# Performance work log

Hardware: AMD Instinct MI355X
Metric: run time of the kernel (lower is better)

## Reference

```python
import jax, jax.numpy as jnp
import numpy as np
from jax import lax

B, L = 4, 1024
D_MODEL = 512
D_INNER = 2 * D_MODEL            # expand=2 -> 1024
HEADDIM = 64
NHEADS = D_INNER // HEADDIM      # 16
D_STATE = 64
D_CONV = 4
NLAYERS = 2
NTOKEN = 60695
PAD_IDX = 60694
NCLS = 164
CONV_DIM = D_INNER + 2 * D_STATE            # 1152 (ngroups=1)
D_IN_PROJ = 2 * D_INNER + 2 * D_STATE + NHEADS  # 2192
MAX_VALUE = 512.0
EPS = 1e-5


def _ln(x, g=None, b=None):
    m = jnp.mean(x, -1, keepdims=True)
    v = jnp.mean((x - m) ** 2, -1, keepdims=True)
    y = (x - m) * lax.rsqrt(v + EPS)
    return y if g is None else y * g + b


def _smart_flip(X, pad_mask):
    # reverse only the valid (non-pad) prefix of each sequence
    lengths = (~pad_mask).sum(1)
    rng = jnp.arange(X.shape[1])[None, :]
    flip = rng < lengths[:, None]
    pos = jnp.where(flip, lengths[:, None] - 1 - rng, rng)
    return jnp.take_along_axis(X, pos[:, :, None], axis=1)


def _mamba2(u, in_w, conv_w, conv_b, A_log, dt_bias, Dskip, norm_w, out_w):
    # Mamba2 block (mamba_ssm defaults: ngroups=1, silu conv act, gated RMSNorm)
    Bb, Ll, _ = u.shape
    zxbcdt = u @ in_w.T                                      # (B,L,D_IN_PROJ)
    z = zxbcdt[..., :D_INNER]
    xBC = zxbcdt[..., D_INNER:D_INNER + CONV_DIM]
    dt = jax.nn.softplus(zxbcdt[..., -NHEADS:] + dt_bias)    # (B,L,H)
    # causal depthwise conv1d + silu
    xBC = jnp.pad(xBC, ((0, 0), (D_CONV - 1, 0), (0, 0))).transpose(0, 2, 1)
    xBC = lax.conv_general_dilated(xBC, conv_w[:, None, :], (1,), 'VALID',
                                   feature_group_count=CONV_DIM)
    xBC = jax.nn.silu(xBC.transpose(0, 2, 1) + conv_b)       # (B,L,CONV_DIM)
    x = xBC[..., :D_INNER].reshape(Bb, Ll, NHEADS, HEADDIM)
    Bm = xBC[..., D_INNER:D_INNER + D_STATE]                 # (B,L,N)
    Cm = xBC[..., D_INNER + D_STATE:]                        # (B,L,N)
    dA = jnp.exp(dt * (-jnp.exp(A_log)))                     # (B,L,H)

    def step(h, t):
        dA_t, dt_t, x_t, B_t, C_t = t
        # h: (B,H,P,N)
        h = h * dA_t[:, :, None, None] \
            + (dt_t[:, :, None] * x_t)[..., None] * B_t[:, None, None, :]
        y = jnp.einsum('bhpn,bn->bhp', h, C_t)
        return h, y

    h0 = jnp.zeros((Bb, NHEADS, HEADDIM, D_STATE), u.dtype)
    xs = (dA.transpose(1, 0, 2), dt.transpose(1, 0, 2),
          x.transpose(1, 0, 2, 3), Bm.transpose(1, 0, 2), Cm.transpose(1, 0, 2))
    _, ys = lax.scan(step, h0, xs)                            # (L,B,H,P)
    y = ys.transpose(1, 0, 2, 3) + Dskip[None, None, :, None] * x
    y = y.reshape(Bb, Ll, D_INNER)
    y = y * jax.nn.silu(z)                                    # gated RMSNorm
    y = y * lax.rsqrt(jnp.mean(y * y, -1, keepdims=True) + EPS) * norm_w
    return y @ out_w.T


def _forward(src, values, pad_mask, embed, ge_ln_g, ge_ln_b,
             ve_w1, ve_b1, ve_w2, ve_b2, ve_ln_g, ve_ln_b,
             in_proj_w, conv_w_f, conv_b_f, A_log_f, dt_bias_f, D_f, norm_w_f,
             conv_w_r, conv_b_r, A_log_r, dt_bias_r, D_r, norm_w_r, out_proj_w,
             expr_w1, expr_b1, expr_w2, expr_b2, expr_w3, expr_b3,
             cls_w1, cls_b1, cls_ln1_g, cls_ln1_b, cls_w2, cls_b2,
             cls_ln2_g, cls_ln2_b, cls_wo, cls_bo):
    src_emb = _ln(embed[src], ge_ln_g, ge_ln_b)
    v = jnp.minimum(values, MAX_VALUE)[..., None]
    v = jax.nn.relu(v @ ve_w1.T + ve_b1)
    v = _ln(v @ ve_w2.T + ve_b2, ve_ln_g, ve_ln_b)
    h = (src_emb + v) * (~pad_mask)[..., None]
    for i in range(NLAYERS):
        hn = _ln(h)  # F.layer_norm without affine
        out = _mamba2(hn, in_proj_w[i], conv_w_f[i], conv_b_f[i], A_log_f[i],
                      dt_bias_f[i], D_f[i], norm_w_f[i], out_proj_w[i])
        rev = _smart_flip(hn, pad_mask)
        out_r = _mamba2(rev, in_proj_w[i], conv_w_r[i], conv_b_r[i], A_log_r[i],
                        dt_bias_r[i], D_r[i], norm_w_r[i], out_proj_w[i])
        out_r = _smart_flip(out_r, pad_mask)
        h = _ln((out + out_r) / 2)
    # ExprDecoder (MLM head)
    e = jax.nn.leaky_relu(h @ expr_w1.T + expr_b1)
    e = jax.nn.leaky_relu(e @ expr_w2.T + expr_b2)
    mlm = (e @ expr_w3.T + expr_b3)[..., 0]
    # cell embedding: cls token
    cell = h[:, 0, :]
    # ClsDecoder
    c = _ln(jax.nn.relu(cell @ cls_w1.T + cls_b1), cls_ln1_g, cls_ln1_b)
    c = _ln(jax.nn.relu(c @ cls_w2.T + cls_b2), cls_ln2_g, cls_ln2_b)
    cls = c @ cls_wo.T + cls_bo
    return mlm, cell, cls


def setup_inputs() -> dict:
    key = jax.random.key(0)
    ks = iter(jax.random.split(key, 64))
    w = lambda *s: jax.random.normal(next(ks), s, jnp.float32) * 0.02
    embed = w(NTOKEN, D_MODEL).at[PAD_IDX].set(0.0)
    dt_u = jax.random.uniform(next(ks), (NLAYERS, NHEADS), minval=1e-3, maxval=0.1)
    dt_u2 = jax.random.uniform(next(ks), (NLAYERS, NHEADS), minval=1e-3, maxval=0.1)
    return dict(
        src=jax.random.randint(next(ks), (B, L), 0, PAD_IDX),
        values=jax.random.uniform(next(ks), (B, L), jnp.float32),
        src_key_padding_mask=jnp.zeros((B, L), bool),
        embed=embed,
        ge_ln_g=jnp.ones((D_MODEL,)), ge_ln_b=jnp.zeros((D_MODEL,)),
        ve_w1=w(D_MODEL, 1), ve_b1=jnp.zeros((D_MODEL,)),
        ve_w2=w(D_MODEL, D_MODEL), ve_b2=jnp.zeros((D_MODEL,)),
        ve_ln_g=jnp.ones((D_MODEL,)), ve_ln_b=jnp.zeros((D_MODEL,)),
        in_proj_w=w(NLAYERS, D_IN_PROJ, D_MODEL),
        conv_w_f=w(NLAYERS, CONV_DIM, D_CONV), conv_b_f=jnp.zeros((NLAYERS, CONV_DIM)),
        A_log_f=jnp.log(jax.random.uniform(next(ks), (NLAYERS, NHEADS), minval=1.0, maxval=16.0)),
        dt_bias_f=dt_u + jnp.log(-jnp.expm1(-dt_u)),
        D_f=jnp.ones((NLAYERS, NHEADS)), norm_w_f=jnp.ones((NLAYERS, D_INNER)),
        conv_w_r=w(NLAYERS, CONV_DIM, D_CONV), conv_b_r=jnp.zeros((NLAYERS, CONV_DIM)),
        A_log_r=jnp.log(jax.random.uniform(next(ks), (NLAYERS, NHEADS), minval=1.0, maxval=16.0)),
        dt_bias_r=dt_u2 + jnp.log(-jnp.expm1(-dt_u2)),
        D_r=jnp.ones((NLAYERS, NHEADS)), norm_w_r=jnp.ones((NLAYERS, D_INNER)),
        out_proj_w=w(NLAYERS, D_MODEL, D_INNER),
        expr_w1=w(D_MODEL, D_MODEL), expr_b1=jnp.zeros((D_MODEL,)),
        expr_w2=w(D_MODEL, D_MODEL), expr_b2=jnp.zeros((D_MODEL,)),
        expr_w3=w(1, D_MODEL), expr_b3=jnp.zeros((1,)),
        cls_w1=w(D_MODEL, D_MODEL), cls_b1=jnp.zeros((D_MODEL,)),
        cls_ln1_g=jnp.ones((D_MODEL,)), cls_ln1_b=jnp.zeros((D_MODEL,)),
        cls_w2=w(D_MODEL, D_MODEL), cls_b2=jnp.zeros((D_MODEL,)),
        cls_ln2_g=jnp.ones((D_MODEL,)), cls_ln2_b=jnp.zeros((D_MODEL,)),
        cls_wo=w(NCLS, D_MODEL), cls_bo=jnp.zeros((NCLS,)),
    )


def reference(src, values, src_key_padding_mask, embed, ge_ln_g, ge_ln_b,
              ve_w1, ve_b1, ve_w2, ve_b2, ve_ln_g, ve_ln_b,
              in_proj_w, conv_w_f, conv_b_f, A_log_f, dt_bias_f, D_f, norm_w_f,
              conv_w_r, conv_b_r, A_log_r, dt_bias_r, D_r, norm_w_r, out_proj_w,
              expr_w1, expr_b1, expr_w2, expr_b2, expr_w3, expr_b3,
              cls_w1, cls_b1, cls_ln1_g, cls_ln1_b, cls_w2, cls_b2,
              cls_ln2_g, cls_ln2_b, cls_wo, cls_bo):
    return _forward(src, values, src_key_padding_mask, embed, ge_ln_g, ge_ln_b,
                    ve_w1, ve_b1, ve_w2, ve_b2, ve_ln_g, ve_ln_b,
                    in_proj_w, conv_w_f, conv_b_f, A_log_f, dt_bias_f, D_f, norm_w_f,
                    conv_w_r, conv_b_r, A_log_r, dt_bias_r, D_r, norm_w_r, out_proj_w,
                    expr_w1, expr_b1, expr_w2, expr_b2, expr_w3, expr_b3,
                    cls_w1, cls_b1, cls_ln1_g, cls_ln1_b, cls_w2, cls_b2,
                    cls_ln2_g, cls_ln2_b, cls_wo, cls_bo)
```

## Files before the change

kernel.cpp:

```cpp
#include <hip/hip_runtime.h>
#include <hip/hip_bf16.h>
#include <math.h>

constexpr int Bb = 4, Ls = 1024, DM = 512, DI = 1024, NH = 16, HD = 64, DS = 64;
constexpr int CDIM = DI + 2 * DS;
constexpr int DIP  = 2 * DI + 2 * DS + NH;
constexpr int NPJ  = 2 * DI + 2 * DS;
constexpr float EPSf = 1e-5f;
constexpr int TOK = Bb * Ls;
constexpr int CH = 64, NCH = Ls / CH;

#define DEVI __device__ __forceinline__

using bfrag = __attribute__((ext_vector_type(8))) short;
using f4v   = __attribute__((ext_vector_type(4))) float;
using u16x8 = __attribute__((ext_vector_type(8))) unsigned short;

#define GLOAD16(gp, lp)                                                              \
  __builtin_amdgcn_global_load_lds((__attribute__((address_space(1))) void*)(gp),   \
                                   (__attribute__((address_space(3))) void*)(lp),   \
                                   16, 0, 0)

DEVI float wsum(float v) {
#pragma unroll
  for (int o = 32; o > 0; o >>= 1) v += __shfl_xor(v, o);
  return v;
}
DEVI float sigmoidf_(float x) { return 1.f / (1.f + __expf(-x)); }
DEVI unsigned short f2bf(float x) {
  union { float f; unsigned u; } c{x};
  unsigned u = c.u;
  u += 0x7fffu + ((u >> 16) & 1u);
  return (unsigned short)(u >> 16);
}
DEVI float bf2f(unsigned short u) {
  union { unsigned u; float f; } c{(unsigned)u << 16};
  return c.f;
}

DEVI void ld8(const float* __restrict__ p, int lane, float (&x)[8]) {
  float4 a = *(const float4*)(p + lane * 4);
  float4 b = *(const float4*)(p + 256 + lane * 4);
  x[0] = a.x; x[1] = a.y; x[2] = a.z; x[3] = a.w;
  x[4] = b.x; x[5] = b.y; x[6] = b.z; x[7] = b.w;
}
DEVI void ld8bf(const unsigned short* __restrict__ p, int lane, float (&x)[8]) {
  ushort4 a = *(const ushort4*)(p + lane * 4);
  ushort4 b = *(const ushort4*)(p + 256 + lane * 4);
  x[0] = bf2f(a.x); x[1] = bf2f(a.y); x[2] = bf2f(a.z); x[3] = bf2f(a.w);
  x[4] = bf2f(b.x); x[5] = bf2f(b.y); x[6] = bf2f(b.z); x[7] = bf2f(b.w);
}
DEVI void st8(float* __restrict__ p, int lane, const float (&x)[8]) {
  *(float4*)(p + lane * 4) = make_float4(x[0], x[1], x[2], x[3]);
  *(float4*)(p + 256 + lane * 4) = make_float4(x[4], x[5], x[6], x[7]);
}
DEVI void st8bf(unsigned short* __restrict__ p, int lane, const float (&x)[8]) {
  *(ushort4*)(p + lane * 4) = make_ushort4(f2bf(x[0]), f2bf(x[1]), f2bf(x[2]), f2bf(x[3]));
  *(ushort4*)(p + 256 + lane * 4) = make_ushort4(f2bf(x[4]), f2bf(x[5]), f2bf(x[6]), f2bf(x[7]));
}
DEVI void norm8(float (&x)[8]) {
  float s = 0;
#pragma unroll
  for (int j = 0; j < 8; ++j) s += x[j];
  float mean = wsum(s) * (1.f / 512.f);
#pragma unroll
  for (int j = 0; j < 8; ++j) x[j] -= mean;
  float q = 0;
#pragma unroll
  for (int j = 0; j < 8; ++j) q += x[j] * x[j];
  float var = wsum(q) * (1.f / 512.f);
  float inv = rsqrtf(var + EPSf);
#pragma unroll
  for (int j = 0; j < 8; ++j) x[j] *= inv;
}

__global__ __launch_bounds__(256) void k_w2bf(const float* __restrict__ in,
                                              unsigned short* __restrict__ out, int n8) {
  int i = blockIdx.x * 256 + threadIdx.x;
  if (i >= n8) return;
  const float4* p = (const float4*)in + (size_t)i * 2;
  float4 a = p[0], b = p[1];
  *((ushort4*)out + (size_t)i * 2) = make_ushort4(f2bf(a.x), f2bf(a.y), f2bf(a.z), f2bf(a.w));
  *((ushort4*)out + (size_t)i * 2 + 1) = make_ushort4(f2bf(b.x), f2bf(b.y), f2bf(b.z), f2bf(b.w));
}

__global__ __launch_bounds__(256) void k_embed(const int* __restrict__ src, const float* __restrict__ values,
    const float* __restrict__ embed, const float* __restrict__ gg, const float* __restrict__ gb,
    const float* __restrict__ vw1, const float* __restrict__ vb1,
    float* __restrict__ hbuf, unsigned short* __restrict__ v1bf) {
  int gw = (blockIdx.x * 256 + threadIdx.x) >> 6;
  int lane = threadIdx.x & 63;
  if (gw >= TOK) return;
  const float* er = embed + (size_t)src[gw] * DM;
  float x[8];
  ld8(er, lane, x);
  norm8(x);
  float g[8], bv[8];
  ld8(gg, lane, g); ld8(gb, lane, bv);
#pragma unroll
  for (int j = 0; j < 8; ++j) x[j] = x[j] * g[j] + bv[j];
  st8(hbuf + (size_t)gw * DM, lane, x);
  float val = fminf(values[gw], 512.f);
  float w1[8], b1[8];
  ld8(vw1, lane, w1); ld8(vb1, lane, b1);
  float v[8];
#pragma unroll
  for (int j = 0; j < 8; ++j) v[j] = fmaxf(val * w1[j] + b1[j], 0.f);
  st8bf(v1bf + (size_t)gw * DM, lane, v);
}

__global__ __launch_bounds__(256) void k_haddv(const float* __restrict__ t2, const float* __restrict__ g,
    const float* __restrict__ bb, const unsigned char* __restrict__ mask, float* __restrict__ hbuf) {
  int gw = (blockIdx.x * 256 + threadIdx.x) >> 6;
  int lane = threadIdx.x & 63;
  if (gw >= TOK) return;
  float x[8];
  ld8(t2 + (size_t)gw * DM, lane, x);
  norm8(x);
  float gv[8], bv[8], h[8];
  ld8(g, lane, gv); ld8(bb, lane, bv);
  ld8(hbuf + (size_t)gw * DM, lane, h);
  float mf = mask[gw] ? 0.f : 1.f;
#pragma unroll
  for (int j = 0; j < 8; ++j) h[j] = (h[j] + x[j] * gv[j] + bv[j]) * mf;
  st8(hbuf + (size_t)gw * DM, lane, h);
}

__global__ __launch_bounds__(256) void k_lndt(const float* __restrict__ h, const float* __restrict__ inw,
    const float* __restrict__ dtbF, const float* __restrict__ AlogF,
    const float* __restrict__ dtbR, const float* __restrict__ AlogR,
    const int* __restrict__ len, unsigned short* __restrict__ hnbf,
    float* __restrict__ dtf, float* __restrict__ laf,
    float* __restrict__ dtr, float* __restrict__ lar) {
  int gw = (blockIdx.x * 256 + threadIdx.x) >> 6;
  int lane = threadIdx.x & 63;
  if (gw >= TOK) return;
  float x[8];
  ld8(h + (size_t)gw * DM, lane, x);
  norm8(x);
  st8bf(hnbf + (size_t)gw * DM, lane, x);
  const float* wdt = inw + (size_t)NPJ * DM;
  float myraw = 0.f;
#pragma unroll
  for (int hh = 0; hh < NH; ++hh) {
    float w[8];
    ld8(wdt + (size_t)hh * DM, lane, w);
    float s = 0;
#pragma unroll
    for (int j = 0; j < 8; ++j) s += x[j] * w[j];
    s = wsum(s);
    if (lane == hh) myraw = s;
  }
  if (lane < NH) {
    int t = gw & (Ls - 1), b = gw >> 10;
    int ln = len[b];
    int pos = (t < ln) ? (ln - 1 - t) : t;
    size_t grev = (size_t)(b * Ls + pos);
    float rf = myraw + dtbF[lane];
    float df = rf > 20.f ? rf : log1pf(__expf(rf));
    dtf[(size_t)gw * NH + lane] = df;
    laf[(size_t)gw * NH + lane] = -__expf(AlogF[lane]) * df;
    float rr = myraw + dtbR[lane];
    float dr = rr > 20.f ? rr : log1pf(__expf(rr));
    dtr[grev * NH + lane] = dr;
    lar[grev * NH + lane] = -__expf(AlogR[lane]) * dr;
  }
}

template <int ACT, int OMODE>
__global__ __launch_bounds__(256) void gemm_bf(const unsigned short* __restrict__ A,
    const unsigned short* __restrict__ W, const float* __restrict__ bias,
    void* __restrict__ Cout, int M, int N, int K) {
  constexpr int BK = 64;
  __shared__ unsigned short As[128 * BK];
  __shared__ unsigned short Bs[128 * BK];
  int tid = threadIdx.x;
  int bm = blockIdx.y * 128, bn = blockIdx.x * 128;
  int wv = tid >> 6, lane = tid & 63;
  int mb = (wv >> 1) * 64, nb = (wv & 1) * 64;
  int rA = lane >> 3;
  int cswz = (lane & 7) ^ rA;
  f4v acc[4][4] = {};

  for (int k0 = 0; k0 < K; k0 += BK) {
#pragma unroll
    for (int q = 0; q < 4; ++q) {
      int ch = wv * 4 + q;
      const unsigned short* ga = A + (size_t)(bm + ch * 8 + rA) * K + k0 + cswz * 8;
      GLOAD16(ga, &As[ch * 512]);
      const unsigned short* gb = W + (size_t)(bn + ch * 8 + rA) * K + k0 + cswz * 8;
      GLOAD16(gb, &Bs[ch * 512]);
    }
    __syncthreads();
#pragma unroll
    for (int ks = 0; ks < BK; ks += 32) {
      int kb = (ks >> 3) + (lane >> 4);
      bfrag af[4], bg[4];
#pragma unroll
      for (int i = 0; i < 4; ++i) {
        int ra_ = mb + i * 16 + (lane & 15);
        af[i] = *(const bfrag*)((const char*)As + ((ra_ * 128 + kb * 16) ^ ((ra_ & 7) << 4)));
        int rb_ = nb + i * 16 + (lane & 15);
        bg[i] = *(const bfrag*)((const char*)Bs + ((rb_ * 128 + kb * 16) ^ ((rb_ & 7) << 4)));
      }
#pragma unroll
      for (int i = 0; i < 4; ++i)
#pragma unroll
        for (int j = 0; j < 4; ++j)
          acc[i][j] = __builtin_amdgcn_mfma_f32_16x16x32_bf16(af[i], bg[j], acc[i][j], 0, 0, 0);
    }
    __syncthreads();
  }

  int cb = bn + nb + (lane & 15);
  int rb = bm + mb + ((lane >> 4) << 2);
#pragma unroll
  for (int j = 0; j < 4; ++j) {
    float bv = bias ? bias[cb + j * 16] : 0.f;
#pragma unroll
    for (int i = 0; i < 4; ++i) {
#pragma unroll
      for (int r = 0; r < 4; ++r) {
        float v = acc[i][j][r] + bv;
        if (ACT == 1) v = fmaxf(v, 0.f);
        if (ACT == 2) v = v > 0.f ? v : 0.01f * v;
        size_t idx = (size_t)(rb + i * 16 + r) * N + cb + j * 16;
        if (OMODE == 0) ((float*)Cout)[idx] = v;
        else ((unsigned short*)Cout)[idx] = f2bf(v);
      }
    }
  }
}

__global__ __launch_bounds__(256) void k_chunk(const unsigned short* __restrict__ zx,
    const float* __restrict__ cwF, const float* __restrict__ cbF,
    const float* __restrict__ cwR, const float* __restrict__ cbR,
    const float* __restrict__ dtF, const float* __restrict__ laF,
    const float* __restrict__ dtR, const float* __restrict__ laR,
    const float* __restrict__ DkF, const float* __restrict__ DkR,
    const int* __restrict__ len,
    float* __restrict__ yF, float* __restrict__ yR,
    float* __restrict__ gbuf, float* __restrict__ cumbuf, unsigned short* __restrict__ cbuf) {
  __shared__ unsigned short Cb[4096], Bbs[4096], BbT[4096], xT[4096], Wt[4096];
  __shared__ float ldsL[64], sdt_[64], fs[64];
  int blk2 = blockIdx.x;
  int dir = blk2 >> 10;
  int blk = blk2 & 1023;
  int c = blk & 15, bh = blk >> 4, h = bh & 15, b = bh >> 4;
  int tid = threadIdx.x, wv = tid >> 6, lane = tid & 63;
  int c0 = c * CH;
  int ln = len[b];
  const float* cw = dir ? cwR : cwF;
  const float* cbias = dir ? cbR : cbF;
  const float* dtp = dir ? dtR : dtF;
  const float* ldap = dir ? laR : laF;
  float Dh = (dir ? DkR : DkF)[h];
  float* y = dir ? yR : yF;

  if (tid < 64) {
    size_t off = ((size_t)(b * Ls + c0 + tid)) * NH + h;
    float dtv = dtp[off];
    float v = ldap[off];
#pragma unroll
    for (int o = 1; o < 64; o <<= 1) {
      float n = __shfl_up(v, o);
      if (tid >= o) v += n;
    }
    ldsL[tid] = v;
    sdt_[tid] = dtv;
    cumbuf[(size_t)blk2 * 64 + tid] = __expf(v);
    float L63 = __shfl(v, 63);
    fs[tid] = __expf(L63 - v) * dtv;
  }
  __syncthreads();

  for (int u = tid; u < 768; u += 256) {
    int cch = u % 192, tg = (u / 192) * 16;
    int gcol = cch < 64 ? DI + h * 64 + cch : 2 * DI + (cch - 64);
    int ccd = cch < 64 ? h * 64 + cch : DI + (cch - 64);
    float4 w4 = *(const float4*)(cw + ccd * 4);
    float bias = cbias[ccd];
    float vv[19];
#pragma unroll
    for (int k = 0; k < 19; ++k) {
      int rl = c0 + tg - 3 + k;
      float val = 0.f;
      if (rl >= 0) {
        int gr = dir ? (rl < ln ? ln - 1 - rl : rl) : rl;
        val = bf2f(zx[((size_t)(b * Ls + gr)) * NPJ + gcol]);
      }
      vv[k] = val;
    }
    float o16[16];
#pragma unroll
    for (int t = 0; t < 16; ++t) {
      float s = bias + w4.x * vv[t] + w4.y * vv[t + 1] + w4.z * vv[t + 2] + w4.w * vv[t + 3];
      o16[t] = s * sigmoidf_(s);
    }
    if (cch < 64) {
      int p = cch;
#pragma unroll
      for (int hv = 0; hv < 2; ++hv) {
        u16x8 pk;
#pragma unroll
        for (int k = 0; k < 8; ++k) pk[k] = f2bf(o16[hv * 8 + k]);
        *(u16x8*)((char*)xT + ((p * 128 + (tg + hv * 8) * 2) ^ ((p & 7) << 4))) = pk;
      }
    } else if (cch < 128) {
      int n = cch - 64;
#pragma unroll
      for (int t = 0; t < 16; ++t) {
        int s = tg + t;
        *(unsigned short*)((char*)Bbs + ((s * 128 + n * 2) ^ ((s & 7) << 4))) = f2bf(o16[t]);
      }
#pragma unroll
      for (int hv = 0; hv < 2; ++hv) {
        u16x8 pk;
#pragma unroll
        for (int k = 0; k < 8; ++k) pk[k] = f2bf(o16[hv * 8 + k] * fs[tg + hv * 8 + k]);
        *(u16x8*)((char*)BbT + ((n * 128 + (tg + hv * 8) * 2) ^ ((n & 7) << 4))) = pk;
      }
    } else {
      int n = cch - 128;
#pragma unroll
      for (int t = 0; t < 16; ++t) {
        int s = tg + t;
        *(unsigned short*)((char*)Cb + ((s * 128 + n * 2) ^ ((s & 7) << 4))) = f2bf(o16[t]);
      }
    }
  }
  __syncthreads();

  {
    const u16x8* srcp = (const u16x8*)Cb;
    u16x8* dstp = (u16x8*)(cbuf + (size_t)blk2 * 4096);
    dstp[tid * 2] = srcp[tid * 2];
    dstp[tid * 2 + 1] = srcp[tid * 2 + 1];
  }

  f4v accS[4] = {};
#pragma unroll
  for (int ks = 0; ks < 64; ks += 32) {
    int kb = (ks >> 3) + (lane >> 4);
    int ra = wv * 16 + (lane & 15);
    bfrag af = *(const bfrag*)((const char*)Cb + ((ra * 128 + kb * 16) ^ ((ra & 7) << 4)));
#pragma unroll
    for (int j = 0; j < 4; ++j) {
      int rb = j * 16 + (lane & 15);
      bfrag bg = *(const bfrag*)((const char*)Bbs + ((rb * 128 + kb * 16) ^ ((rb & 7) << 4)));
      accS[j] = __builtin_amdgcn_mfma_f32_16x16x32_bf16(af, bg, accS[j], 0, 0, 0);
    }
  }
  {
    int trow = wv * 16 + ((lane >> 4) << 2);
#pragma unroll
    for (int j = 0; j < 4; ++j) {
      int s = j * 16 + (lane & 15);
      float ds = sdt_[s], Lsv = ldsL[s];
#pragma unroll
      for (int r = 0; r < 4; ++r) {
        int tt = trow + r;
        float wval = (s <= tt) ? accS[j][r] * ds * __expf(ldsL[tt] - Lsv) : 0.f;
        *(unsigned short*)((char*)Wt + ((tt * 128 + s * 2) ^ ((tt & 7) << 4))) = f2bf(wval);
      }
    }
  }
  __syncthreads();

  f4v accY[4] = {}, accG[4] = {};
#pragma unroll
  for (int ks = 0; ks < 64; ks += 32) {
    int kb = (ks >> 3) + (lane >> 4);
    int ra = wv * 16 + (lane & 15);
    bfrag afW = *(const bfrag*)((const char*)Wt + ((ra * 128 + kb * 16) ^ ((ra & 7) << 4)));
    bfrag afB = *(const bfrag*)((const char*)BbT + ((ra * 128 + kb * 16) ^ ((ra & 7) << 4)));
#pragma unroll
    for (int j = 0; j < 4; ++j) {
      int rb = j * 16 + (lane & 15);
      bfrag bg = *(const bfrag*)((const char*)xT + ((rb * 128 + kb * 16) ^ ((rb & 7) << 4)));
      accY[j] = __builtin_amdgcn_mfma_f32_16x16x32_bf16(afW, bg, accY[j], 0, 0, 0);
      accG[j] = __builtin_amdgcn_mfma_f32_16x16x32_bf16(afB, bg, accG[j], 0, 0, 0);
    }
  }
  int trow = wv * 16 + ((lane >> 4) << 2);
#pragma unroll
  for (int j = 0; j < 4; ++j) {
    int p = j * 16 + (lane & 15);
#pragma unroll
    for (int r = 0; r < 4; ++r) {
      int t = trow + r;
      float xval = bf2f(*(const unsigned short*)((const char*)xT + ((p * 128 + t * 2) ^ ((p & 7) << 4))));
      y[((size_t)(b * Ls + c0 + t)) * DI + h * 64 + p] = accY[j][r] + Dh * xval;
      gbuf[((size_t)blk2 * 64 + t) * 64 + p] = accG[j][r];
    }
  }
}

__global__ __launch_bounds__(256) void k_chain(float* __restrict__ gbuf, const float* __restrict__ cumbuf) {
  int bh = blockIdx.x;
  int tid = threadIdx.x;
  size_t base = (size_t)bh * NCH * 4096;
  float4 hv[4] = {};
  float4 g[4], gn[4];
#pragma unroll
  for (int k = 0; k < 4; ++k) g[k] = *(const float4*)(gbuf + base + (size_t)k * 1024 + tid * 4);
  float Pc = cumbuf[(size_t)bh * NCH * 64 + 63];
  for (int c = 0; c < NCH; ++c) {
    float Pn = 0.f;
    if (c + 1 < NCH) {
      Pn = cumbuf[((size_t)bh * NCH + c + 1) * 64 + 63];
#pragma unroll
      for (int k = 0; k < 4; ++k)
        gn[k] = *(const float4*)(gbuf + base + (size_t)(c + 1) * 4096 + (size_t)k * 1024 + tid * 4);
    }
#pragma unroll
    for (int k = 0; k < 4; ++k) {
      *(float4*)(gbuf + base + (size_t)c * 4096 + (size_t)k * 1024 + tid * 4) = hv[k];
      hv[k].x = fmaf(Pc, hv[k].x, g[k].x);
      hv[k].y = fmaf(Pc, hv[k].y, g[k].y);
      hv[k].z = fmaf(Pc, hv[k].z, g[k].z);
      hv[k].w = fmaf(Pc, hv[k].w, g[k].w);
      g[k] = gn[k];
    }
    Pc = Pn;
  }
}

__global__ __launch_bounds__(256) void k_corr(const unsigned short* __restrict__ cbuf,
    const float* __restrict__ hin, const float* __restrict__ cumbuf,
    float* __restrict__ yF, float* __restrict__ yR) {
  int blk2 = blockIdx.x;
  int c = blk2 & 15;
  if (c == 0) return;
  __shared__ unsigned short Ct[4096], HT[4096];
  __shared__ float cdl[64];
  int dir = blk2 >> 10;
  int bh = (blk2 & 1023) >> 4, h = bh & 15, b = bh >> 4;
  int tid = threadIdx.x, wv = tid >> 6, lane = tid & 63;
  int c0 = c * CH;
  float* y = dir ? yR : yF;
  {
    const unsigned short* g = cbuf + (size_t)blk2 * 4096;
#pragma unroll
    for (int q = 0; q < 2; ++q)
      GLOAD16(g + wv * 1024 + q * 512 + lane * 8, &Ct[wv * 1024 + q * 512]);
  }
  {
    int n = tid >> 2, p0 = (tid & 3) * 16;
    const float* hr = hin + (size_t)blk2 * 4096 + (size_t)n * 64 + p0;
#pragma unroll
    for (int q = 0; q < 4; ++q) {
      float4 v = *(const float4*)(hr + q * 4);
      float va[4] = {v.x, v.y, v.z, v.w};
#pragma unroll
      for (int k = 0; k < 4; ++k) {
        int p = p0 + q * 4 + k;
        *(unsigned short*)((char*)HT + ((p * 128 + n * 2) ^ ((p & 7) << 4))) = f2bf(va[k]);
      }
    }
  }
  if (tid < 64) cdl[tid] = cumbuf[(size_t)blk2 * 64 + tid];
  __syncthreads();

  f4v acc[4] = {};
#pragma unroll
  for (int ks = 0; ks < 64; ks += 32) {
    int kb = (ks >> 3) + (lane >> 4);
    int ra = wv * 16 + (lane & 15);
    bfrag af = *(const bfrag*)((const char*)Ct + ((ra * 128 + kb * 16) ^ ((ra & 7) << 4)));
#pragma unroll
    for (int j = 0; j < 4; ++j) {
      int rb = j * 16 + (lane & 15);
      bfrag bg = *(const bfrag*)((const char*)HT + ((rb * 128 + kb * 16) ^ ((rb & 7) << 4)));
      acc[j] = __builtin_amdgcn_mfma_f32_16x16x32_bf16(af, bg, acc[j], 0, 0, 0);
    }
  }
  int trow = wv * 16 + ((lane >> 4) << 2);
#pragma unroll
  for (int j = 0; j < 4; ++j) {
    int p = j * 16 + (lane & 15);
#pragma unroll
    for (int r = 0; r < 4; ++r) {
      int t = trow + r;
      float* yp = &y[((size_t)(b * Ls + c0 + t)) * DI + h * 64 + p];
      *yp += cdl[t] * acc[j][r];
    }
  }
}

__global__ __launch_bounds__(256) void k_gab(const float* __restrict__ yF, const float* __restrict__ yR,
    const unsigned short* __restrict__ zxb, const float* __restrict__ nwF, const float* __restrict__ nwR,
    const int* __restrict__ len, unsigned short* __restrict__ ybf) {
  int w = (blockIdx.x * 256 + threadIdx.x) >> 6;
  int lane = threadIdx.x & 63;
  if (w >= TOK) return;
  int t = w & (Ls - 1), b = w >> 10;
  int ln = len[b];
  int r = b * Ls + ((t < ln) ? (ln - 1 - t) : t);
  const float* yf = yF + (size_t)w * DI;
  const float* yr = yR + (size_t)r * DI;
  const unsigned short* zr = zxb + (size_t)w * NPJ;
  float gf[16], gr[16];
  float ssf = 0.f, ssr = 0.f;
#pragma unroll
  for (int q = 0; q < 4; ++q) {
    float4 yv = *(const float4*)(yf + lane * 4 + q * 256);
    float4 rv = *(const float4*)(yr + lane * 4 + q * 256);
    ushort4 zu = *(const ushort4*)(zr + lane * 4 + q * 256);
    float z0 = bf2f(zu.x), z1 = bf2f(zu.y), z2 = bf2f(zu.z), z3 = bf2f(zu.w);
    float s0 = z0 * sigmoidf_(z0), s1 = z1 * sigmoidf_(z1), s2 = z2 * sigmoidf_(z2), s3 = z3 * sigmoidf_(z3);
    gf[4 * q + 0] = yv.x * s0; gf[4 * q + 1] = yv.y * s1; gf[4 * q + 2] = yv.z * s2; gf[4 * q + 3] = yv.w * s3;
    gr[4 * q + 0] = rv.x * s0; gr[4 * q + 1] = rv.y * s1; gr[4 * q + 2] = rv.z * s2; gr[4 * q + 3] = rv.w * s3;
#pragma unroll
    for (int j = 0; j < 4; ++j) {
      ssf += gf[4 * q + j] * gf[4 * q + j];
      ssr += gr[4 * q + j] * gr[4 * q + j];
    }
  }
  ssf = wsum(ssf);
  ssr = wsum(ssr);
  float scf = 0.5f * rsqrtf(ssf * (1.f / (float)DI) + EPSf);
  float scr = 0.5f * rsqrtf(ssr * (1.f / (float)DI) + EPSf);
#pragma unroll
  for (int q = 0; q < 4; ++q) {
    float4 nf = *(const float4*)(nwF + lane * 4 + q * 256);
    float4 nr = *(const float4*)(nwR + lane * 4 + q * 256);
    float o0 = gf[4 * q + 0] * scf * nf.x + gr[4 * q + 0] * scr * nr.x;
    float o1 = gf[4 * q + 1] * scf * nf.y + gr[4 * q + 1] * scr * nr.y;
    float o2 = gf[4 * q + 2] * scf * nf.z + gr[4 * q + 2] * scr * nr.z;
    float o3 = gf[4 * q + 3] * scf * nf.w + gr[4 * q + 3] * scr * nr.w;
    *(ushort4*)(ybf + (size_t)w * DI + lane * 4 + q * 256) =
        make_ushort4(f2bf(o0), f2bf(o1), f2bf(o2), f2bf(o3));
  }
}

__global__ __launch_bounds__(256) void k_hln(const float* __restrict__ src, float* __restrict__ dst,
                                             unsigned short* __restrict__ dstbf) {
  int gw = (blockIdx.x * 256 + threadIdx.x) >> 6;
  int lane = threadIdx.x & 63;
  if (gw >= TOK) return;
  float x[8];
  ld8(src + (size_t)gw * DM, lane, x);
  norm8(x);
  st8(dst + (size_t)gw * DM, lane, x);
  st8bf(dstbf + (size_t)gw * DM, lane, x);
}

__global__ __launch_bounds__(256) void k_lengths(const unsigned char* __restrict__ mask, int* __restrict__ len) {
  int b = blockIdx.x;
  int tid = threadIdx.x;
  int cnt = 0;
  for (int t = tid; t < Ls; t += 256) cnt += mask[b * Ls + t] ? 0 : 1;
#pragma unroll
  for (int o = 32; o > 0; o >>= 1) cnt += __shfl_xor(cnt, o);
  __shared__ int red[4];
  if ((tid & 63) == 0) red[tid >> 6] = cnt;
  __syncthreads();
  if (tid == 0) len[b] = red[0] + red[1] + red[2] + red[3];
}

__global__ __launch_bounds__(256) void k_mlm(const unsigned short* __restrict__ e2,
                                             const float* __restrict__ w3,
                                             const float* __restrict__ b3, float* __restrict__ out) {
  int gw = (blockIdx.x * 256 + threadIdx.x) >> 6;
  int lane = threadIdx.x & 63;
  if (gw >= TOK) return;
  float x[8], w[8];
  ld8bf(e2 + (size_t)gw * DM, lane, x);
  ld8(w3, lane, w);
  float s = 0;
#pragma unroll
  for (int j = 0; j < 8; ++j) s += x[j] * w[j];
  s = wsum(s);
  if (lane == 0) out[gw] = s + b3[0];
}

__global__ __launch_bounds__(256) void k_cell(const float* __restrict__ h, float* __restrict__ out) {
  int i = blockIdx.x * 256 + threadIdx.x;
  if (i >= Bb * DM) return;
  int b = i >> 9, c = i & 511;
  out[i] = h[(size_t)b * Ls * DM + c];
}

__global__ __launch_bounds__(256) void k_clsmv(const float* __restrict__ xin, size_t xstride,
    const float* __restrict__ g, const float* __restrict__ bb, int doLN,
    const float* __restrict__ W, const float* __restrict__ bias, int doRelu,
    float* __restrict__ out, int nout) {
  int b = blockIdx.y;
  int j = blockIdx.x * 4 + (threadIdx.x >> 6);
  int lane = threadIdx.x & 63;
  if (j >= nout) return;
  float x[8];
  ld8(xin + (size_t)b * xstride, lane, x);
  if (doLN) {
    norm8(x);
    float gv[8], bv[8];
    ld8(g, lane, gv); ld8(bb, lane, bv);
#pragma unroll
    for (int k = 0; k < 8; ++k) x[k] = x[k] * gv[k] + bv[k];
  }
  float w[8];
  ld8(W + (size_t)j * DM, lane, w);
  float s = 0;
#pragma unroll
  for (int k = 0; k < 8; ++k) s += x[k] * w[k];
  s = wsum(s);
  if (lane == 0) {
    float v = s + bias[j];
    if (doRelu) v = fmaxf(v, 0.f);
    out[(size_t)b * nout + j] = v;
  }
}

constexpr size_t F_H   = 0;
constexpr size_t F_DTF = F_H + (size_t)TOK * DM;
constexpr size_t F_LAF = F_DTF + (size_t)TOK * NH;
constexpr size_t F_DTR = F_LAF + (size_t)TOK * NH;
constexpr size_t F_LAR = F_DTR + (size_t)TOK * NH;
constexpr size_t F_YF  = F_LAR + (size_t)TOK * NH;
constexpr size_t F_YR  = F_YF + (size_t)TOK * DI;
constexpr size_t F_ON  = F_YR + (size_t)TOK * DI;
constexpr size_t F_G   = F_ON + (size_t)TOK * DM;
constexpr size_t F_CUM = F_G + (size_t)2 * Bb * NH * NCH * HD * DS;
constexpr size_t F_CC1 = F_CUM + (size_t)2 * Bb * NH * NCH * 64;
constexpr size_t F_CC2 = F_CC1 + Bb * DM;
constexpr size_t F_LEN = F_CC2 + Bb * DM;
constexpr size_t F_END = F_LEN + 16;
constexpr size_t U0     = F_END * 2;
constexpr size_t UW_IN  = U0;
constexpr size_t UW_OUT = UW_IN + (size_t)2 * DIP * DM;
constexpr size_t UW_VE  = UW_OUT + (size_t)2 * DM * DI;
constexpr size_t UW_E1  = UW_VE + (size_t)DM * DM;
constexpr size_t UW_E2  = UW_E1 + (size_t)DM * DM;
constexpr size_t U_BFA  = UW_E2 + (size_t)DM * DM;
constexpr size_t U_HNBF = U_BFA + (size_t)TOK * DM;
constexpr size_t U_YBF  = U_HNBF + (size_t)TOK * DM;
constexpr size_t U_ZX   = U_YBF + (size_t)TOK * DI;
constexpr size_t U_CBUF = U_ZX + (size_t)TOK * NPJ;

extern "C" void kernel_launch(void* const* d_in, const int* in_sizes, int n_in,
                              void* d_out, int out_size, void* d_ws, size_t ws_size,
                              hipStream_t stream) {
  const int* src = (const int*)d_in[0];
  const float* values = (const float*)d_in[1];
  const unsigned char* mask = (const unsigned char*)d_in[2];
  const float* embed = (const float*)d_in[3];
  const float* ge_g = (const float*)d_in[4];
  const float* ge_b = (const float*)d_in[5];
  const float* ve_w1 = (const float*)d_in[6];
  const float* ve_b1 = (const float*)d_in[7];
  const float* ve_w2 = (const float*)d_in[8];
  const float* ve_b2 = (const float*)d_in[9];
  const float* ve_g = (const float*)d_in[10];
  const float* ve_bb = (const float*)d_in[11];
  const float* in_w = (const float*)d_in[12];
  const float* conv_w_f = (const float*)d_in[13];
  const float* conv_b_f = (const float*)d_in[14];
  const float* A_f = (const float*)d_in[15];
  const float* dtb_f = (const float*)d_in[16];
  const float* D_f = (const float*)d_in[17];
  const float* nw_f = (const float*)d_in[18];
  const float* conv_w_r = (const float*)d_in[19];
  const float* conv_b_r = (const float*)d_in[20];
  const float* A_r = (const float*)d_in[21];
  const float* dtb_r = (const float*)d_in[22];
  const float* D_r = (const float*)d_in[23];
  const float* nw_r = (const float*)d_in[24];
  const float* out_w = (const float*)d_in[25];
  const float* expr_w1 = (const float*)d_in[26];
  const float* expr_b1 = (const float*)d_in[27];
  const float* expr_w2 = (const float*)d_in[28];
  const float* expr_b2 = (const float*)d_in[29];
  const float* expr_w3 = (const float*)d_in[30];
  const float* expr_b3 = (const float*)d_in[31];
  const float* cls_w1 = (const float*)d_in[32];
  const float* cls_b1 = (const float*)d_in[33];
  const float* cls_g1 = (const float*)d_in[34];
  const float* cls_bb1 = (const float*)d_in[35];
  const float* cls_w2 = (const float*)d_in[36];
  const float* cls_b2 = (const float*)d_in[37];
  const float* cls_g2 = (const float*)d_in[38];
  const float* cls_bb2 = (const float*)d_in[39];
  const float* cls_wo = (const float*)d_in[40];
  const float* cls_bo = (const float*)d_in[41];

  float* ws = (float*)d_ws;
  unsigned short* wsu = (unsigned short*)d_ws;
  float* h = ws + F_H;
  float* dtf = ws + F_DTF;
  float* laf = ws + F_LAF;
  float* dtr = ws + F_DTR;
  float* lar = ws + F_LAR;
  float* yF = ws + F_YF;
  float* yR = ws + F_YR;
  float* onew = ws + F_ON;
  float* gbuf = ws + F_G;
  float* cumb = ws + F_CUM;
  float* cc1 = ws + F_CC1;
  float* cc2 = ws + F_CC2;
  int* len = (int*)(ws + F_LEN);
  unsigned short* w_in = wsu + UW_IN;
  unsigned short* w_out = wsu + UW_OUT;
  unsigned short* w_ve = wsu + UW_VE;
  unsigned short* w_e1 = wsu + UW_E1;
  unsigned short* w_e2 = wsu + UW_E2;
  unsigned short* bfa = wsu + U_BFA;
  unsigned short* hnbf = wsu + U_HNBF;
  unsigned short* ybf = wsu + U_YBF;
  unsigned short* zxb = wsu + U_ZX;
  unsigned short* cbuf = wsu + U_CBUF;
  float* t2 = onew;
  unsigned short* e2b = zxb;
  float* out = (float*)d_out;

  {
    int n;
    n = 2 * DIP * DM / 8;  k_w2bf<<<(n + 255) / 256, 256, 0, stream>>>(in_w, w_in, n);
    n = 2 * DM * DI / 8;   k_w2bf<<<(n + 255) / 256, 256, 0, stream>>>(out_w, w_out, n);
    n = DM * DM / 8;       k_w2bf<<<(n + 255) / 256, 256, 0, stream>>>(ve_w2, w_ve, n);
    n = DM * DM / 8;       k_w2bf<<<(n + 255) / 256, 256, 0, stream>>>(expr_w1, w_e1, n);
    n = DM * DM / 8;       k_w2bf<<<(n + 255) / 256, 256, 0, stream>>>(expr_w2, w_e2, n);
  }

  k_embed<<<TOK / 4, 256, 0, stream>>>(src, values, embed, ge_g, ge_b, ve_w1, ve_b1, h, bfa);
  gemm_bf<0, 0><<<dim3(DM / 128, TOK / 128), 256, 0, stream>>>(bfa, w_ve, ve_b2, t2, TOK, DM, DM);
  k_haddv<<<TOK / 4, 256, 0, stream>>>(t2, ve_g, ve_bb, mask, h);
  k_lengths<<<Bb, 256, 0, stream>>>(mask, len);

  for (int i = 0; i < 2; ++i) {
    const float* inw = in_w + (size_t)i * DIP * DM;
    unsigned short* inwb = w_in + (size_t)i * DIP * DM;
    unsigned short* outwb = w_out + (size_t)i * DM * DI;
    k_lndt<<<TOK / 4, 256, 0, stream>>>(h, inw, dtb_f + i * NH, A_f + i * NH,
                                        dtb_r + i * NH, A_r + i * NH, len, hnbf,
                                        dtf, laf, dtr, lar);
    gemm_bf<0, 1><<<dim3(NPJ / 128, TOK / 128), 256, 0, stream>>>(hnbf, inwb, nullptr, zxb, TOK, NPJ, DM);
    k_chunk<<<2 * Bb * NH * NCH, 256, 0, stream>>>(zxb,
        conv_w_f + (size_t)i * CDIM * 4, conv_b_f + (size_t)i * CDIM,
        conv_w_r + (size_t)i * CDIM * 4, conv_b_r + (size_t)i * CDIM,
        dtf, laf, dtr, lar, D_f + i * NH, D_r + i * NH, len,
        yF, yR, gbuf, cumb, cbuf);
    k_chain<<<2 * Bb * NH, 256, 0, stream>>>(gbuf, cumb);
    k_corr<<<2 * Bb * NH * NCH, 256, 0, stream>>>(cbuf, gbuf, cumb, yF, yR);
    k_gab<<<TOK / 4, 256, 0, stream>>>(yF, yR, zxb, nw_f + (size_t)i * DI, nw_r + (size_t)i * DI,
                                       len, ybf);
    gemm_bf<0, 0><<<dim3(DM / 128, TOK / 128), 256, 0, stream>>>(ybf, outwb, nullptr, onew, TOK, DM, DI);
    k_hln<<<TOK / 4, 256, 0, stream>>>(onew, h, hnbf);
  }

  gemm_bf<2, 1><<<dim3(DM / 128, TOK / 128), 256, 0, stream>>>(hnbf, w_e1, expr_b1, bfa, TOK, DM, DM);
  gemm_bf<2, 1><<<dim3(DM / 128, TOK / 128), 256, 0, stream>>>(bfa, w_e2, expr_b2, e2b, TOK, DM, DM);
  k_mlm<<<TOK / 4, 256, 0, stream>>>(e2b, expr_w3, expr_b3, out);
  k_cell<<<(Bb * DM + 255) / 256, 256, 0, stream>>>(h, out + TOK);
  k_clsmv<<<dim3(128, Bb), 256, 0, stream>>>(h, (size_t)Ls * DM, nullptr, nullptr, 0,
                                             cls_w1, cls_b1, 1, cc1, DM);
  k_clsmv<<<dim3(128, Bb), 256, 0, stream>>>(cc1, DM, cls_g1, cls_bb1, 1,
                                             cls_w2, cls_b2, 1, cc2, DM);
  k_clsmv<<<dim3(41, Bb), 256, 0, stream>>>(cc2, DM, cls_g2, cls_bb2, 1,
                                            cls_wo, cls_bo, 0, out + TOK + Bb * DM, 164);
}
```

Before: 366.6 us.

## Precompute shared B/C conv once per token instead of per head

Adds a k_convbc kernel that runs the depthwise conv and SiLU for the B and C channels once per token and direction, writing bf16 to a buffer. Previously every one of the 16 head blocks recomputed the same B/C conv for its chunk. k_chunk now loads B/C from that buffer and only convolves its own x channels, and k_corr reads C from the same buffer instead of a per-block C copy. This trades redundant conv work for an extra kernel launch and an extra global round trip of the B/C data.

```diff
diff --git a/kernel.cpp b/kernel.cpp
--- a/kernel.cpp
+++ b/kernel.cpp
@@ -232,7 +232,37 @@
   }
 }
 
+__global__ __launch_bounds__(256) void k_convbc(const unsigned short* __restrict__ zx,
+    const float* __restrict__ cwF, const float* __restrict__ cbF,
+    const float* __restrict__ cwR, const float* __restrict__ cbR,
+    const int* __restrict__ len, unsigned short* __restrict__ bcbuf) {
+  int idx = blockIdx.x * 256 + threadIdx.x;
+  if (idx >= 2 * TOK * 128) return;
+  int col = idx & 127;
+  int bt = (idx >> 7) & (TOK - 1);
+  int dir = idx >> 19;
+  int b = bt >> 10, t = bt & (Ls - 1);
+  int ln = len[b];
+  const float* cw = dir ? cwR : cwF;
+  const float* cb = dir ? cbR : cbF;
+  int ccd = DI + col;
+  float4 w4 = *(const float4*)(cw + ccd * 4);
+  float s = cb[ccd];
+  float wk[4] = {w4.x, w4.y, w4.z, w4.w};
+#pragma unroll
+  for (int k = 0; k < 4; ++k) {
+    int rl = t - 3 + k;
+    if (rl >= 0) {
+      int gr = dir ? (rl < ln ? ln - 1 - rl : rl) : rl;
+      s += wk[k] * bf2f(zx[((size_t)(b * Ls + gr)) * NPJ + 2 * DI + col]);
+    }
+  }
+  s = s * sigmoidf_(s);
+  bcbuf[idx] = f2bf(s);
+}
+
 __global__ __launch_bounds__(256) void k_chunk(const unsigned short* __restrict__ zx,
+    const unsigned short* __restrict__ bcbuf,
     const float* __restrict__ cwF, const float* __restrict__ cbF,
     const float* __restrict__ cwR, const float* __restrict__ cbR,
     const float* __restrict__ dtF, const float* __restrict__ laF,
@@ -240,7 +270,7 @@
     const float* __restrict__ DkF, const float* __restrict__ DkR,
     const int* __restrict__ len,
     float* __restrict__ yF, float* __restrict__ yR,
-    float* __restrict__ gbuf, float* __restrict__ cumbuf, unsigned short* __restrict__ cbuf) {
+    float* __restrict__ gbuf, float* __restrict__ cumbuf) {
   __shared__ unsigned short Cb[4096], Bbs[4096], BbT[4096], xT[4096], Wt[4096];
   __shared__ float ldsL[64], sdt_[64], fs[64];
   int blk2 = blockIdx.x;
@@ -274,10 +304,45 @@
   }
   __syncthreads();
 
-  for (int u = tid; u < 768; u += 256) {
-    int cch = u % 192, tg = (u / 192) * 16;
-    int gcol = cch < 64 ? DI + h * 64 + cch : 2 * DI + (cch - 64);
-    int ccd = cch < 64 ? h * 64 + cch : DI + (cch - 64);
+  {
+    const unsigned short* bc = bcbuf + ((size_t)(dir * TOK + b * Ls + c0)) * 128;
+    int r = tid >> 2;
+    int colq = (tid & 3) * 32;
+#pragma unroll
+    for (int g = 0; g < 2; ++g) {
+      int col = colq + g * 16;
+      u16x8 v0 = *(const u16x8*)(bc + (size_t)r * 128 + col);
+      u16x8 v1 = *(const u16x8*)(bc + (size_t)r * 128 + col + 8);
+      if (col < 64) {
+        *(u16x8*)((char*)Bbs + ((r * 128 + col * 2) ^ ((r & 7) << 4))) = v0;
+        *(u16x8*)((char*)Bbs + ((r * 128 + col * 2 + 16) ^ ((r & 7) << 4))) = v1;
+      } else {
+        int n = col - 64;
+        *(u16x8*)((char*)Cb + ((r * 128 + n * 2) ^ ((r & 7) << 4))) = v0;
+        *(u16x8*)((char*)Cb + ((r * 128 + n * 2 + 16) ^ ((r & 7) << 4))) = v1;
+      }
+    }
+  }
+  {
+    int n = tid & 63;
+    int tg = (tid >> 6) * 16;
+    const unsigned short* bc = bcbuf + ((size_t)(dir * TOK + b * Ls + c0 + tg)) * 128 + n;
+    float vals[16];
+#pragma unroll
+    for (int t = 0; t < 16; ++t) vals[t] = bf2f(bc[(size_t)t * 128]) * fs[tg + t];
+#pragma unroll
+    for (int hv = 0; hv < 2; ++hv) {
+      u16x8 pk;
+#pragma unroll
+      for (int k = 0; k < 8; ++k) pk[k] = f2bf(vals[hv * 8 + k]);
+      *(u16x8*)((char*)BbT + ((n * 128 + (tg + hv * 8) * 2) ^ ((n & 7) << 4))) = pk;
+    }
+  }
+  {
+    int cch = tid & 63;
+    int tg = (tid >> 6) * 16;
+    int gcol = DI + h * 64 + cch;
+    int ccd = h * 64 + cch;
     float4 w4 = *(const float4*)(cw + ccd * 4);
     float bias = cbias[ccd];
     float vv[19];
@@ -291,52 +356,20 @@
       }
       vv[k] = val;
     }
-    float o16[16];
-#pragma unroll
-    for (int t = 0; t < 16; ++t) {
-      float s = bias + w4.x * vv[t] + w4.y * vv[t + 1] + w4.z * vv[t + 2] + w4.w * vv[t + 3];
-      o16[t] = s * sigmoidf_(s);
-    }
-    if (cch < 64) {
-      int p = cch;
-#pragma unroll
-      for (int hv = 0; hv < 2; ++hv) {
-        u16x8 pk;
-#pragma unroll
-        for (int k = 0; k < 8; ++k) pk[k] = f2bf(o16[hv * 8 + k]);
-        *(u16x8*)((char*)xT + ((p * 128 + (tg + hv * 8) * 2) ^ ((p & 7) << 4))) = pk;
+    int p = cch;
+#pragma unroll
+    for (int hv = 0; hv < 2; ++hv) {
+      u16x8 pk;
+#pragma unroll
+      for (int k = 0; k < 8; ++k) {
+        int t = hv * 8 + k;
+        float s = bias + w4.x * vv[t] + w4.y * vv[t + 1] + w4.z * vv[t + 2] + w4.w * vv[t + 3];
+        pk[k] = f2bf(s * sigmoidf_(s));
       }
-    } else if (cch < 128) {
-      int n = cch - 64;
-#pragma unroll
-      for (int t = 0; t < 16; ++t) {
-        int s = tg + t;
-        *(unsigned short*)((char*)Bbs + ((s * 128 + n * 2) ^ ((s & 7) << 4))) = f2bf(o16[t]);
-      }
-#pragma unroll
-      for (int hv = 0; hv < 2; ++hv) {
-        u16x8 pk;
-#pragma unroll
-        for (int k = 0; k < 8; ++k) pk[k] = f2bf(o16[hv * 8 + k] * fs[tg + hv * 8 + k]);
-        *(u16x8*)((char*)BbT + ((n * 128 + (tg + hv * 8) * 2) ^ ((n & 7) << 4))) = pk;
-      }
-    } else {
-      int n = cch - 128;
-#pragma unroll
-      for (int t = 0; t < 16; ++t) {
-        int s = tg + t;
-        *(unsigned short*)((char*)Cb + ((s * 128 + n * 2) ^ ((s & 7) << 4))) = f2bf(o16[t]);
-      }
+      *(u16x8*)((char*)xT + ((p * 128 + (tg + hv * 8) * 2) ^ ((p & 7) << 4))) = pk;
     }
   }
   __syncthreads();
-
-  {
-    const u16x8* srcp = (const u16x8*)Cb;
-    u16x8* dstp = (u16x8*)(cbuf + (size_t)blk2 * 4096);
-    dstp[tid * 2] = srcp[tid * 2];
-    dstp[tid * 2 + 1] = srcp[tid * 2 + 1];
-  }
 
   f4v accS[4] = {};
 #pragma unroll
@@ -426,7 +459,7 @@
   }
 }
 
-__global__ __launch_bounds__(256) void k_corr(const unsigned short* __restrict__ cbuf,
+__global__ __launch_bounds__(256) void k_corr(const unsigned short* __restrict__ bcbuf,
     const float* __restrict__ hin, const float* __restrict__ cumbuf,
     float* __restrict__ yF, float* __restrict__ yR) {
   int blk2 = blockIdx.x;
@@ -440,10 +473,13 @@
   int c0 = c * CH;
   float* y = dir ? yR : yF;
   {
-    const unsigned short* g = cbuf + (size_t)blk2 * 4096;
-#pragma unroll
-    for (int q = 0; q < 2; ++q)
-      GLOAD16(g + wv * 1024 + q * 512 + lane * 8, &Ct[wv * 1024 + q * 512]);
+    int r = tid >> 2;
+    int colq = (tid & 3) * 16;
+    const unsigned short* bc = bcbuf + ((size_t)(dir * TOK + b * Ls + c0 + r)) * 128 + 64 + colq;
+    u16x8 v0 = *(const u16x8*)bc;
+    u16x8 v1 = *(const u16x8*)(bc + 8);
+    *(u16x8*)((char*)Ct + ((r * 128 + colq * 2) ^ ((r & 7) << 4))) = v0;
+    *(u16x8*)((char*)Ct + ((r * 128 + colq * 2 + 16) ^ ((r & 7) << 4))) = v1;
   }
   {
     int n = tid >> 2, p0 = (tid & 3) * 16;
@@ -636,7 +672,7 @@
 constexpr size_t U_HNBF = U_BFA + (size_t)TOK * DM;
 constexpr size_t U_YBF  = U_HNBF + (size_t)TOK * DM;
 constexpr size_t U_ZX   = U_YBF + (size_t)TOK * DI;
-constexpr size_t U_CBUF = U_ZX + (size_t)TOK * NPJ;
+constexpr size_t U_BC   = U_ZX + (size_t)TOK * NPJ;
 
 extern "C" void kernel_launch(void* const* d_in, const int* in_sizes, int n_in,
                               void* d_out, int out_size, void* d_ws, size_t ws_size,
@@ -708,7 +744,7 @@
   unsigned short* hnbf = wsu + U_HNBF;
   unsigned short* ybf = wsu + U_YBF;
   unsigned short* zxb = wsu + U_ZX;
-  unsigned short* cbuf = wsu + U_CBUF;
+  unsigned short* bcbuf = wsu + U_BC;
   float* t2 = onew;
   unsigned short* e2b = zxb;
   float* out = (float*)d_out;
@@ -731,17 +767,19 @@
     const float* inw = in_w + (size_t)i * DIP * DM;
     unsigned short* inwb = w_in + (size_t)i * DIP * DM;
     unsigned short* outwb = w_out + (size_t)i * DM * DI;
+    const float* cwF = conv_w_f + (size_t)i * CDIM * 4;
+    const float* cbF = conv_b_f + (size_t)i * CDIM;
+    const float* cwR = conv_w_r + (size_t)i * CDIM * 4;
+    const float* cbR = conv_b_r + (size_t)i * CDIM;
     k_lndt<<<TOK / 4, 256, 0, stream>>>(h, inw, dtb_f + i * NH, A_f + i * NH,
                                         dtb_r + i * NH, A_r + i * NH, len, hnbf,
                                         dtf, laf, dtr, lar);
     gemm_bf<0, 1><<<dim3(NPJ / 128, TOK / 128), 256, 0, stream>>>(hnbf, inwb, nullptr, zxb, TOK, NPJ, DM);
-    k_chunk<<<2 * Bb * NH * NCH, 256, 0, stream>>>(zxb,
-        conv_w_f + (size_t)i * CDIM * 4, conv_b_f + (size_t)i * CDIM,
-        conv_w_r + (size_t)i * CDIM * 4, conv_b_r + (size_t)i * CDIM,
-        dtf, laf, dtr, lar, D_f + i * NH, D_r + i * NH, len,
-        yF, yR, gbuf, cumb, cbuf);
+    k_convbc<<<(2 * TOK * 128) / 256, 256, 0, stream>>>(zxb, cwF, cbF, cwR, cbR, len, bcbuf);
+    k_chunk<<<2 * Bb * NH * NCH, 256, 0, stream>>>(zxb, bcbuf, cwF, cbF, cwR, cbR,
+        dtf, laf, dtr, lar, D_f + i * NH, D_r + i * NH, len, yF, yR, gbuf, cumb);
     k_chain<<<2 * Bb * NH, 256, 0, stream>>>(gbuf, cumb);
-    k_corr<<<2 * Bb * NH * NCH, 256, 0, stream>>>(cbuf, gbuf, cumb, yF, yR);
+    k_corr<<<2 * Bb * NH * NCH, 256, 0, stream>>>(bcbuf, gbuf, cumb, yF, yR);
     k_gab<<<TOK / 4, 256, 0, stream>>>(yF, yR, zxb, nw_f + (size_t)i * DI, nw_r + (size_t)i * DI,
                                        len, ybf);
     gemm_bf<0, 0><<<dim3(DM / 128, TOK / 128), 256, 0, stream>>>(ybf, outwb, nullptr, onew, TOK, DM, DI);
```

Result: faster. 347.9 us (-5.1%).
